# Optimization experiments

Measured on AMD Instinct MI355X. Metric: run time of the kernel, lower is better.

Reference implementation:

```python
import jax, jax.numpy as jnp
import numpy as np


def gru_step(x, h, W, U, b):
    # Keras GRU, reset_after=True. W:[in,3H] U:[H,3H] b:[2,3H]
    gi = x @ W + b[0]
    gh = h @ U + b[1]
    iz, ir, ih = jnp.split(gi, 3, axis=-1)
    hz, hr, hh = jnp.split(gh, 3, axis=-1)
    z = jax.nn.sigmoid(iz + hz)
    r = jax.nn.sigmoid(ir + hr)
    n = jnp.tanh(ih + r * hh)
    return z * h + (1.0 - z) * n


def gru_seq(x, W, U, b):
    # x: [B,S,in] -> outputs [B,S,H], last state [B,H]; zero initial state
    B = x.shape[0]
    H = U.shape[0]
    h0 = jnp.zeros((B, H), x.dtype)
    def step(h, xt):
        h2 = gru_step(xt, h, W, U, b)
        return h2, h2
    hT, ys = jax.lax.scan(step, h0, jnp.swapaxes(x, 0, 1))
    return jnp.swapaxes(ys, 0, 1), hT


def setup_inputs() -> dict:
    key = jax.random.key(0)
    ks = jax.random.split(key, 24)
    V_en, V_fr, E, H = 32000, 32000, 256, 1024
    B, S = 32, 48
    s = 0.05
    d = {}
    d["inputs"] = jax.random.randint(ks[0], (B, S), 0, V_en, dtype=jnp.int32)
    d["gen_seq_len"] = 32
    d["start_id"] = 1
    d["emb_en"] = jax.random.normal(ks[1], (V_en, E), jnp.float32) * s
    d["emb_fr"] = jax.random.normal(ks[2], (V_fr, E), jnp.float32) * s
    # encoder GRUs: layer0 in=E, layer1 in=H
    d["enc_W0"] = jax.random.normal(ks[3], (E, 3 * H), jnp.float32) * s
    d["enc_U0"] = jax.random.normal(ks[4], (H, 3 * H), jnp.float32) * s
    d["enc_b0"] = jnp.zeros((2, 3 * H), jnp.float32)
    d["enc_W1"] = jax.random.normal(ks[5], (H, 3 * H), jnp.float32) * s
    d["enc_U1"] = jax.random.normal(ks[6], (H, 3 * H), jnp.float32) * s
    d["enc_b1"] = jnp.zeros((2, 3 * H), jnp.float32)
    # decoder GRUs: layer0 in = H(context)+E(embed), layer1 in = H
    d["dec_W0"] = jax.random.normal(ks[7], (H + E, 3 * H), jnp.float32) * s
    d["dec_U0"] = jax.random.normal(ks[8], (H, 3 * H), jnp.float32) * s
    d["dec_b0"] = jnp.zeros((2, 3 * H), jnp.float32)
    d["dec_W1"] = jax.random.normal(ks[9], (H, 3 * H), jnp.float32) * s
    d["dec_U1"] = jax.random.normal(ks[10], (H, 3 * H), jnp.float32) * s
    d["dec_b1"] = jnp.zeros((2, 3 * H), jnp.float32)
    # Bahdanau attention
    d["attn_W1"] = jax.random.normal(ks[11], (H, H), jnp.float32) * s
    d["attn_b1"] = jnp.zeros((H,), jnp.float32)
    d["attn_W2"] = jax.random.normal(ks[12], (H, H), jnp.float32) * s
    d["attn_b2"] = jnp.zeros((H,), jnp.float32)
    d["attn_V"] = jax.random.normal(ks[13], (H, 1), jnp.float32) * s
    d["attn_Vb"] = jnp.zeros((1,), jnp.float32)
    # output projection
    d["fc_W"] = jax.random.normal(ks[14], (H, V_fr), jnp.float32) * s
    d["fc_b"] = jnp.zeros((V_fr,), jnp.float32)
    return d


def reference(inputs, gen_seq_len, start_id, emb_en, emb_fr,
              enc_W0, enc_U0, enc_b0, enc_W1, enc_U1, enc_b1,
              dec_W0, dec_U0, dec_b0, dec_W1, dec_U1, dec_b1,
              attn_W1, attn_b1, attn_W2, attn_b2, attn_V, attn_Vb,
              fc_W, fc_b):
    B = inputs.shape[0]
    H = enc_U0.shape[0]
    V_fr = fc_W.shape[1]
    # ---- encoder ----
    x = emb_en[inputs]                       # [B,S,E]
    x, _ = gru_seq(x, enc_W0, enc_U0, enc_b0)
    enc_out, enc_hidden = gru_seq(x, enc_W1, enc_U1, enc_b1)  # [B,S,H], [B,H]
    # precompute W2(values) (same math as recomputing per step)
    enc_proj = enc_out @ attn_W2 + attn_b2   # [B,S,H]
    zeros_h = jnp.zeros((B, H), jnp.float32)

    def dec_step(carry, _):
        dec_in, hidden = carry
        # Bahdanau attention
        q = hidden @ attn_W1 + attn_b1                          # [B,H]
        score = jnp.tanh(q[:, None, :] + enc_proj) @ attn_V + attn_Vb  # [B,S,1]
        w = jax.nn.softmax(score, axis=1)
        ctx = jnp.sum(w * enc_out, axis=1)                      # [B,H]
        xt = jnp.concatenate([ctx, emb_fr[dec_in]], axis=-1)    # [B,H+E]
        # decoder GRUs with state reset to zero each step (initial_state=None)
        h1 = gru_step(xt, zeros_h, dec_W0, dec_U0, dec_b0)
        h2 = gru_step(h1, zeros_h, dec_W1, dec_U1, dec_b1)
        logits = h2 @ fc_W + fc_b                               # [B,V_fr]
        nxt = jnp.argmax(logits, axis=1).astype(jnp.int32)
        return (nxt, h2), logits

    dec_in0 = jnp.full((B,), start_id, dtype=jnp.int32)
    (_, _), logits_seq = jax.lax.scan(dec_step, (dec_in0, enc_hidden),
                                      None, length=gen_seq_len - 1)
    first = jax.nn.one_hot(dec_in0, V_fr, dtype=jnp.float32)[:, None, :]
    return jnp.concatenate([first, jnp.swapaxes(logits_seq, 0, 1)], axis=1)
```

## Files before the change

### kernel.cpp

```cpp
#include <hip/hip_runtime.h>
#include <math.h>

#define BB 32
#define SS 48
#define HH 1024
#define EE 256
#define VOC 32000
#define GEN 32
#define G3 3072
#define CH 256
#define NLOG (VOC / 128)

typedef float v4f __attribute__((ext_vector_type(4)));

__device__ __forceinline__ float sigf(float x) { return 1.f / (1.f + expf(-x)); }

__global__ __launch_bounds__(256) void embed_en_k(const int* __restrict__ inputs,
                                                  const float* __restrict__ emb,
                                                  float* __restrict__ x) {
    int i = blockIdx.x * 256 + threadIdx.x;
    int row = i >> 8;
    int e = i & 255;
    x[i] = emb[(size_t)inputs[row] * EE + e];
}

__global__ __launch_bounds__(256) void transpose_k(const float* __restrict__ U,
                                                   float* __restrict__ UT,
                                                   int R, int C) {
    __shared__ float t[32][33];
    int tx = threadIdx.x & 31, ty = threadIdx.x >> 5;
    int bx = blockIdx.x * 32;
    int by = blockIdx.y * 32;
#pragma unroll
    for (int i = 0; i < 4; ++i)
        t[ty + 8 * i][tx] = U[(size_t)(by + ty + 8 * i) * C + bx + tx];
    __syncthreads();
#pragma unroll
    for (int i = 0; i < 4; ++i)
        UT[(size_t)(bx + ty + 8 * i) * R + by + tx] = t[tx][ty + 8 * i];
}

__global__ __launch_bounds__(256) void gemm64(const float* __restrict__ A,
                                              const float* __restrict__ Bm,
                                              const float* __restrict__ bias,
                                              float* __restrict__ C,
                                              int N, int K) {
    __shared__ float As[32][68];
    __shared__ float Bs[32][68];
    int tid = threadIdx.x;
    int tx = tid & 15, ty = tid >> 4;
    int arow = blockIdx.y * 64, bcol = blockIdx.x * 64;
    int am = tid >> 2;
    int aq = tid & 3;
    int bk = tid >> 4;
    int bn = tid & 15;
    float acc[4][4] = {};
    for (int k0 = 0; k0 < K; k0 += 32) {
        float4 a0 = *(const float4*)(A + (size_t)(arow + am) * K + k0 + aq * 8);
        float4 a1 = *(const float4*)(A + (size_t)(arow + am) * K + k0 + aq * 8 + 4);
        float4 b0 = *(const float4*)(Bm + (size_t)(k0 + bk) * N + bcol + bn * 4);
        float4 b1 = *(const float4*)(Bm + (size_t)(k0 + bk + 16) * N + bcol + bn * 4);
        __syncthreads();
        As[aq * 8 + 0][am] = a0.x; As[aq * 8 + 1][am] = a0.y;
        As[aq * 8 + 2][am] = a0.z; As[aq * 8 + 3][am] = a0.w;
        As[aq * 8 + 4][am] = a1.x; As[aq * 8 + 5][am] = a1.y;
        As[aq * 8 + 6][am] = a1.z; As[aq * 8 + 7][am] = a1.w;
        *(float4*)&Bs[bk][bn * 4] = b0;
        *(float4*)&Bs[bk + 16][bn * 4] = b1;
        __syncthreads();
#pragma unroll
        for (int kk = 0; kk < 32; ++kk) {
            float4 a = *(const float4*)&As[kk][ty * 4];
            float4 b = *(const float4*)&Bs[kk][tx * 4];
            acc[0][0] += a.x * b.x; acc[0][1] += a.x * b.y;
            acc[0][2] += a.x * b.z; acc[0][3] += a.x * b.w;
            acc[1][0] += a.y * b.x; acc[1][1] += a.y * b.y;
            acc[1][2] += a.y * b.z; acc[1][3] += a.y * b.w;
            acc[2][0] += a.z * b.x; acc[2][1] += a.z * b.y;
            acc[2][2] += a.z * b.z; acc[2][3] += a.z * b.w;
            acc[3][0] += a.w * b.x; acc[3][1] += a.w * b.y;
            acc[3][2] += a.w * b.z; acc[3][3] += a.w * b.w;
        }
    }
    float4 bb = *(const float4*)&bias[bcol + tx * 4];
#pragma unroll
    for (int i = 0; i < 4; ++i) {
        size_t row = arow + ty * 4 + i;
        *(float4*)(C + row * N + bcol + tx * 4) =
            make_float4(acc[i][0] + bb.x, acc[i][1] + bb.y,
                        acc[i][2] + bb.z, acc[i][3] + bb.w);
    }
}

__global__ __launch_bounds__(384) void enc_step(
    const float* __restrict__ gi,
    const float* __restrict__ UT,
    const float* __restrict__ b1,
    const float* __restrict__ hin,
    float* __restrict__ hout,
    float* __restrict__ seqout,
    int t) {
    __shared__ float hs[32][260];
    __shared__ float ghs[12][33];
    const int tid = threadIdx.x;
    const int c0 = blockIdx.x * 4;
    const int ks = tid & 31;
    const int outIdx = tid >> 5;
    const int cq = outIdx >> 2;
    const int mo = outIdx & 3;
    const float* Ubase = UT + (size_t)(cq * HH + c0) * HH;
    float acc[4][8];
#pragma unroll
    for (int a = 0; a < 4; ++a)
#pragma unroll
        for (int b = 0; b < 8; ++b) acc[a][b] = 0.f;
    for (int ch = 0; ch < HH / CH; ++ch) {
        for (int i = tid; i < 32 * 64; i += 384) {
            int m = i >> 6, q = i & 63;
            *(float4*)&hs[m][q * 4] =
                *(const float4*)&hin[m * HH + ch * CH + q * 4];
        }
        __syncthreads();
#pragma unroll
        for (int j = 0; j < 2; ++j) {
            int kq = (j * 32 + ks) * 4;
            float4 uv[4];
#pragma unroll
            for (int ci = 0; ci < 4; ++ci)
                uv[ci] = *(const float4*)&Ubase[(size_t)ci * HH + ch * CH + kq];
#pragma unroll
            for (int mi = 0; mi < 8; ++mi) {
                float4 hv = *(const float4*)&hs[mo * 8 + mi][kq];
#pragma unroll
                for (int ci = 0; ci < 4; ++ci)
                    acc[ci][mi] += hv.x * uv[ci].x + hv.y * uv[ci].y +
                                   hv.z * uv[ci].z + hv.w * uv[ci].w;
            }
        }
        __syncthreads();
    }
#pragma unroll
    for (int ci = 0; ci < 4; ++ci)
#pragma unroll
        for (int mi = 0; mi < 8; ++mi) {
            float v = acc[ci][mi];
            v += __shfl_xor(v, 1, 64);
            v += __shfl_xor(v, 2, 64);
            v += __shfl_xor(v, 4, 64);
            v += __shfl_xor(v, 8, 64);
            v += __shfl_xor(v, 16, 64);
            if (ks == 0) ghs[cq * 4 + ci][mo * 8 + mi] = v;
        }
    __syncthreads();
    if (tid < 128) {
        int m = tid & 31, c = tid >> 5;
        int col = c0 + c;
        float ghz = ghs[c][m] + b1[col];
        float ghr = ghs[4 + c][m] + b1[HH + col];
        float ghh = ghs[8 + c][m] + b1[2 * HH + col];
        const float* gir = gi + ((size_t)m * SS + t) * G3;
        float z = sigf(gir[col] + ghz);
        float r = sigf(gir[HH + col] + ghr);
        float nn = tanhf(gir[2 * HH + col] + r * ghh);
        float h = z * hin[m * HH + col] + (1.f - z) * nn;
        hout[m * HH + col] = h;
        seqout[((size_t)m * SS + t) * HH + col] = h;
    }
}

__global__ __launch_bounds__(384) void dec_step(
    const float* __restrict__ xt, int K,
    const float* __restrict__ WT,
    const float* __restrict__ b0, const float* __restrict__ b1,
    float* __restrict__ hout) {
    __shared__ float hs[32][260];
    __shared__ float ghs[12][33];
    const int tid = threadIdx.x;
    const int c0 = blockIdx.x * 4;
    const int ks = tid & 31;
    const int outIdx = tid >> 5;
    const int cq = outIdx >> 2;
    const int mo = outIdx & 3;
    const float* Ubase = WT + (size_t)(cq * HH + c0) * K;
    float acc[4][8];
#pragma unroll
    for (int a = 0; a < 4; ++a)
#pragma unroll
        for (int b = 0; b < 8; ++b) acc[a][b] = 0.f;
    const int nch = K / CH;
    for (int ch = 0; ch < nch; ++ch) {
        for (int i = tid; i < 32 * 64; i += 384) {
            int m = i >> 6, q = i & 63;
            *(float4*)&hs[m][q * 4] =
                *(const float4*)&xt[(size_t)m * K + ch * CH + q * 4];
        }
        __syncthreads();
#pragma unroll
        for (int j = 0; j < 2; ++j) {
            int kq = (j * 32 + ks) * 4;
            float4 uv[4];
#pragma unroll
            for (int ci = 0; ci < 4; ++ci)
                uv[ci] = *(const float4*)&Ubase[(size_t)ci * K + ch * CH + kq];
#pragma unroll
            for (int mi = 0; mi < 8; ++mi) {
                float4 hv = *(const float4*)&hs[mo * 8 + mi][kq];
#pragma unroll
                for (int ci = 0; ci < 4; ++ci)
                    acc[ci][mi] += hv.x * uv[ci].x + hv.y * uv[ci].y +
                                   hv.z * uv[ci].z + hv.w * uv[ci].w;
            }
        }
        __syncthreads();
    }
#pragma unroll
    for (int ci = 0; ci < 4; ++ci)
#pragma unroll
        for (int mi = 0; mi < 8; ++mi) {
            float v = acc[ci][mi];
            v += __shfl_xor(v, 1, 64);
            v += __shfl_xor(v, 2, 64);
            v += __shfl_xor(v, 4, 64);
            v += __shfl_xor(v, 8, 64);
            v += __shfl_xor(v, 16, 64);
            if (ks == 0) ghs[cq * 4 + ci][mo * 8 + mi] = v;
        }
    __syncthreads();
    if (tid < 128) {
        int m = tid & 31, c = tid >> 5;
        int col = c0 + c;
        float z = sigf(ghs[c][m] + b0[col] + b1[col]);
        float r = sigf(ghs[4 + c][m] + b0[HH + col] + b1[HH + col]);
        float nn = tanhf(ghs[8 + c][m] + b0[2 * HH + col] + r * b1[2 * HH + col]);
        hout[m * HH + col] = (1.f - z) * nn;
    }
}

__global__ __launch_bounds__(384) void dec_front(
    const float* __restrict__ qb, const float* __restrict__ encP,
    const float* __restrict__ vvec, const float* __restrict__ vb,
    const float* __restrict__ emb_fr, const int* __restrict__ start_id,
    const float* __restrict__ pmv, const int* __restrict__ pmi, int nb,
    const float* __restrict__ P, const float* __restrict__ W0,
    const float* __restrict__ b0, const float* __restrict__ b1,
    float* __restrict__ h1out) {
    __shared__ float sc[SS];
    __shared__ float wsm[SS];
    __shared__ float sv[256];
    __shared__ int si[256];
    __shared__ int stok;
    __shared__ float embl[EE];
    __shared__ float g[3][128];
    const int tid = threadIdx.x;
    const int b = blockIdx.x & 31;
    const int j0 = (blockIdx.x >> 5) * 128;
    const int wave = tid >> 6, lane = tid & 63;
    if (nb == 0) {
        if (tid == 0) stok = start_id[0];
    } else {
        if (tid < 256) {
            float best = -3.4e38f; int bi = 0x7fffffff;
            for (int i = tid; i < nb; i += 256) {
                float v = pmv[(size_t)b * nb + i];
                int ix = pmi[(size_t)b * nb + i];
                if (v > best || (v == best && ix < bi)) { best = v; bi = ix; }
            }
            sv[tid] = best; si[tid] = bi;
        }
        __syncthreads();
        for (int s = 128; s; s >>= 1) {
            if (tid < s) {
                if (sv[tid + s] > sv[tid] ||
                    (sv[tid + s] == sv[tid] && si[tid + s] < si[tid])) {
                    sv[tid] = sv[tid + s]; si[tid] = si[tid + s];
                }
            }
            __syncthreads();
        }
        if (tid == 0) stok = si[0];
    }
    __syncthreads();
    if (tid < EE) embl[tid] = emb_fr[(size_t)stok * EE + tid];
    const float* q = qb + (size_t)b * HH;
    for (int s = wave; s < SS; s += 6) {
        const float* ep = encP + (size_t)(b * SS + s) * HH;
        float sum = 0.f;
        for (int h = lane; h < HH; h += 64)
            sum += tanhf(q[h] + ep[h]) * vvec[h];
#pragma unroll
        for (int o = 32; o; o >>= 1) sum += __shfl_xor(sum, o, 64);
        if (lane == 0) sc[s] = sum + vb[0];
    }
    __syncthreads();
    if (tid < 64) {
        float v = (lane < SS) ? sc[lane] : -3.4e38f;
        float m = v;
#pragma unroll
        for (int o = 32; o; o >>= 1) m = fmaxf(m, __shfl_xor(m, o, 64));
        float e = (lane < SS) ? expf(v - m) : 0.f;
        float ssum = e;
#pragma unroll
        for (int o = 32; o; o >>= 1) ssum += __shfl_xor(ssum, o, 64);
        if (lane < SS) wsm[lane] = e / ssum;
    }
    __syncthreads();
    {
        int gate = tid >> 7;
        int col = tid & 127;
        int gcol = gate * HH + j0 + col;
        float acc = b0[gcol];
        const float* Pb = P + (size_t)b * SS * G3 + gcol;
#pragma unroll 8
        for (int s = 0; s < SS; ++s) acc += wsm[s] * Pb[(size_t)s * G3];
        const float* Wb = W0 + (size_t)HH * G3 + gcol;
#pragma unroll 8
        for (int k = 0; k < EE; ++k) acc += embl[k] * Wb[(size_t)k * G3];
        g[gate][col] = acc;
    }
    __syncthreads();
    if (tid < 128) {
        int jj = j0 + tid;
        float z = sigf(g[0][tid] + b1[jj]);
        float r = sigf(g[1][tid] + b1[HH + jj]);
        float nn = tanhf(g[2][tid] + r * b1[2 * HH + jj]);
        h1out[(size_t)b * HH + jj] = (1.f - z) * nn;
    }
}

__global__ __launch_bounds__(256) void logits_q(const float* __restrict__ A,
                                                const float* __restrict__ fcW,
                                                const float* __restrict__ fcb,
                                                float* __restrict__ Cl,
                                                const float* __restrict__ qW,
                                                const float* __restrict__ qb,
                                                float* __restrict__ Cq,
                                                float* __restrict__ pmv,
                                                int* __restrict__ pmi,
                                                int qonly) {
    __shared__ float As[32][36];
    __shared__ float Bs[32][132];
    int tid = threadIdx.x;
    int bid = blockIdx.x;
    bool isq = qonly || (bid >= NLOG);
    const float* Bm = isq ? qW : fcW;
    const float* bias = isq ? qb : fcb;
    float* C = isq ? Cq : Cl;
    int N = isq ? HH : VOC;
    int ldc = isq ? HH : GEN * VOC;
    int bcol = (isq ? (qonly ? bid : bid - NLOG) : bid) * 128;
    int nc = tid & 15, mg = (tid >> 4) & 7, ksl = tid >> 7;
    const int nch = HH / 32;
    int am = tid >> 3, aq = tid & 7;
    float4 ra = *(const float4*)(A + (size_t)am * HH + aq * 4);
    float4 rb[4];
#pragma unroll
    for (int it = 0; it < 4; ++it) {
        int lin = it * 256 + tid;
        int k = lin >> 5, q = lin & 31;
        const float* p = Bm + (size_t)k * N + bcol + q * 4;
        if (isq) { rb[it] = *(const float4*)p; }
        else { v4f v = __builtin_nontemporal_load((const v4f*)p); rb[it] = *(float4*)&v; }
    }
    float acc[4][8] = {};
    for (int ch = 0; ch < nch; ++ch) {
        __syncthreads();
        As[aq * 4 + 0][am] = ra.x; As[aq * 4 + 1][am] = ra.y;
        As[aq * 4 + 2][am] = ra.z; As[aq * 4 + 3][am] = ra.w;
#pragma unroll
        for (int it = 0; it < 4; ++it) {
            int lin = it * 256 + tid;
            int k = lin >> 5, q = lin & 31;
            *(float4*)&Bs[k][q * 4] = rb[it];
        }
        __syncthreads();
        if (ch + 1 < nch) {
            int k0 = (ch + 1) * 32;
            ra = *(const float4*)(A + (size_t)am * HH + k0 + aq * 4);
#pragma unroll
            for (int it = 0; it < 4; ++it) {
                int lin = it * 256 + tid;
                int k = lin >> 5, q = lin & 31;
                const float* p = Bm + (size_t)(k0 + k) * N + bcol + q * 4;
                if (isq) { rb[it] = *(const float4*)p; }
                else { v4f v = __builtin_nontemporal_load((const v4f*)p); rb[it] = *(float4*)&v; }
            }
        }
#pragma unroll
        for (int kk = 0; kk < 16; ++kk) {
            int k2 = kk * 2 + ksl;
            float a[4], b[8];
            *(float4*)&a[0] = *(const float4*)&As[k2][mg * 4];
            *(float4*)&b[0] = *(const float4*)&Bs[k2][nc * 8];
            *(float4*)&b[4] = *(const float4*)&Bs[k2][nc * 8 + 4];
#pragma unroll
            for (int r = 0; r < 4; ++r)
#pragma unroll
                for (int j = 0; j < 8; ++j) acc[r][j] += a[r] * b[j];
        }
    }
    __syncthreads();
    float* red = &Bs[0][0];
    if (ksl == 1) {
        int p = tid & 127;
#pragma unroll
        for (int r = 0; r < 4; ++r)
#pragma unroll
            for (int j = 0; j < 8; ++j) red[p * 32 + r * 8 + j] = acc[r][j];
    }
    __syncthreads();
    if (ksl == 0) {
        int p = tid;
#pragma unroll
        for (int r = 0; r < 4; ++r)
#pragma unroll
            for (int j = 0; j < 8; ++j) acc[r][j] += red[p * 32 + r * 8 + j];
        float bb[8];
        *(float4*)&bb[0] = *(const float4*)&bias[bcol + nc * 8];
        *(float4*)&bb[4] = *(const float4*)&bias[bcol + nc * 8 + 4];
#pragma unroll
        for (int r = 0; r < 4; ++r) {
#pragma unroll
            for (int j = 0; j < 8; ++j) acc[r][j] += bb[j];
            int row = mg * 4 + r;
            float* cp = C + (size_t)row * ldc + bcol + nc * 8;
            if (isq) {
                *(float4*)cp = make_float4(acc[r][0], acc[r][1], acc[r][2], acc[r][3]);
                *(float4*)(cp + 4) = make_float4(acc[r][4], acc[r][5], acc[r][6], acc[r][7]);
            } else {
                v4f o0 = {acc[r][0], acc[r][1], acc[r][2], acc[r][3]};
                v4f o1 = {acc[r][4], acc[r][5], acc[r][6], acc[r][7]};
                __builtin_nontemporal_store(o0, (v4f*)cp);
                __builtin_nontemporal_store(o1, (v4f*)(cp + 4));
            }
        }
        if (!isq) {
#pragma unroll
            for (int r = 0; r < 4; ++r) {
                float best = acc[r][0]; int bidx = bcol + nc * 8;
#pragma unroll
                for (int j = 1; j < 8; ++j)
                    if (acc[r][j] > best) { best = acc[r][j]; bidx = bcol + nc * 8 + j; }
#pragma unroll
                for (int o = 1; o < 16; o <<= 1) {
                    float pv = __shfl_xor(best, o, 64);
                    int pi = __shfl_xor(bidx, o, 64);
                    if (pv > best || (pv == best && pi < bidx)) { best = pv; bidx = pi; }
                }
                if (nc == 0) {
                    int row = mg * 4 + r;
                    pmv[row * NLOG + bid] = best;
                    pmi[row * NLOG + bid] = bidx;
                }
            }
        }
    }
}

__global__ __launch_bounds__(256) void init_dec(float* __restrict__ out,
                                                const int* __restrict__ start_id) {
    int idx = blockIdx.x * 256 + threadIdx.x;
    int sid = start_id[0];
    int b = idx / VOC, v = idx % VOC;
    out[(size_t)b * (GEN * VOC) + v] = (v == sid) ? 1.f : 0.f;
}

extern "C" void kernel_launch(void* const* d_in, const int* in_sizes, int n_in,
                              void* d_out, int out_size, void* d_ws, size_t ws_size,
                              hipStream_t stream) {
    const int*   inputs   = (const int*)d_in[0];
    const int*   start_id = (const int*)d_in[2];
    const float* emb_en   = (const float*)d_in[3];
    const float* emb_fr   = (const float*)d_in[4];
    const float* enc_W0   = (const float*)d_in[5];
    const float* enc_U0   = (const float*)d_in[6];
    const float* enc_b0   = (const float*)d_in[7];
    const float* enc_W1   = (const float*)d_in[8];
    const float* enc_U1   = (const float*)d_in[9];
    const float* enc_b1   = (const float*)d_in[10];
    const float* dec_W0   = (const float*)d_in[11];
    const float* dec_b0   = (const float*)d_in[13];
    const float* dec_W1   = (const float*)d_in[14];
    const float* dec_b1   = (const float*)d_in[16];
    const float* attn_W1  = (const float*)d_in[17];
    const float* attn_b1  = (const float*)d_in[18];
    const float* attn_W2  = (const float*)d_in[19];
    const float* attn_b2  = (const float*)d_in[20];
    const float* attn_V   = (const float*)d_in[21];
    const float* attn_Vb  = (const float*)d_in[22];
    const float* fc_W     = (const float*)d_in[23];
    const float* fc_b     = (const float*)d_in[24];
    float* out = (float*)d_out;
    float* ws  = (float*)d_ws;

    float* giA   = ws;
    float* x_emb = giA + (size_t)BB * SS * G3;
    float* seq0  = x_emb + (size_t)BB * SS * EE;
    float* encO  = seq0 + (size_t)BB * SS * HH;
    float* encP  = encO + (size_t)BB * SS * HH;
    float* h0A   = encP + (size_t)BB * SS * HH;
    float* h0B   = h0A + BB * HH;
    float* h1A   = h0B + BB * HH;
    float* h1B   = h1A + BB * HH;
    float* qbuf  = h1B + BB * HH;
    float* h1buf = qbuf + BB * HH;
    float* pmv   = h1buf + BB * HH;
    int*   pmi   = (int*)(pmv + 32 * NLOG);
    float* U0T   = (float*)(pmi + 32 * NLOG);
    float* U1T   = U0T + (size_t)G3 * HH;
    float* Pmat  = giA;
    float* W1Td  = U0T;
    float* zb    = h1B;

    embed_en_k<<<(BB * SS * EE) / 256, 256, 0, stream>>>(inputs, emb_en, x_emb);
    gemm64<<<dim3(G3 / 64, (BB * SS) / 64), 256, 0, stream>>>(
        x_emb, enc_W0, enc_b0, giA, G3, EE);
    transpose_k<<<dim3(96, 32), 256, 0, stream>>>(enc_U0, U0T, HH, G3);
    transpose_k<<<dim3(96, 32), 256, 0, stream>>>(enc_U1, U1T, HH, G3);
    hipMemsetAsync(h0A, 0, BB * HH * sizeof(float), stream);
    for (int t = 0; t < SS; ++t) {
        const float* hin = (t & 1) ? h0B : h0A;
        float* hout = (t & 1) ? h0A : h0B;
        enc_step<<<256, 384, 0, stream>>>(giA, U0T, enc_b0 + G3, hin, hout, seq0, t);
    }
    gemm64<<<dim3(G3 / 64, (BB * SS) / 64), 256, 0, stream>>>(
        seq0, enc_W1, enc_b1, giA, G3, HH);
    hipMemsetAsync(h1A, 0, BB * HH * sizeof(float), stream);
    for (int t = 0; t < SS; ++t) {
        const float* hin = (t & 1) ? h1B : h1A;
        float* hout = (t & 1) ? h1A : h1B;
        enc_step<<<256, 384, 0, stream>>>(giA, U1T, enc_b1 + G3, hin, hout, encO, t);
    }
    gemm64<<<dim3(HH / 64, (BB * SS) / 64), 256, 0, stream>>>(
        encO, attn_W2, attn_b2, encP, HH, HH);

    transpose_k<<<dim3(96, 32), 256, 0, stream>>>(dec_W1, W1Td, HH, G3);
    hipMemsetAsync(zb, 0, G3 * sizeof(float), stream);
    gemm64<<<dim3(G3 / 64, (BB * SS) / 64), 256, 0, stream>>>(
        encO, dec_W0, zb, Pmat, G3, HH);

    init_dec<<<(BB * VOC) / 256, 256, 0, stream>>>(out, start_id);
    logits_q<<<HH / 128, 256, 0, stream>>>(h1A, fc_W, fc_b, out,
                                           attn_W1, attn_b1, qbuf, pmv, pmi, 1);
    for (int step = 1; step < GEN; ++step) {
        dec_front<<<256, 384, 0, stream>>>(qbuf, encP, attn_V, attn_Vb,
                                           emb_fr, start_id, pmv, pmi,
                                           (step == 1) ? 0 : NLOG,
                                           Pmat, dec_W0, dec_b0, dec_b0 + G3,
                                           h1buf);
        dec_step<<<256, 384, 0, stream>>>(h1buf, HH, W1Td, dec_b1,
                                          dec_b1 + G3, h1A);
        logits_q<<<NLOG + HH / 128, 256, 0, stream>>>(h1A, fc_W, fc_b,
                                                      out + (size_t)step * VOC,
                                                      attn_W1, attn_b1, qbuf,
                                                      pmv, pmi, 0);
    }
}
```

Before: 6.995 ms.

## Split logits GEMM into 64-column tiles with 4-way K split and double-buffered prefetch

The vocabulary logits path now uses 64-column tiles, which doubles the block count to 500 and gives better CU coverage on the 32000-wide fc_W stream. Each block splits K four ways and reduces the partial sums through padded shared memory. Register prefetch now runs two chunks ahead to hide more of the global load latency. The attention-query path keeps the old 128-column tiling, and the per-block argmax partials grow to 500 entries per row for dec_front to scan.

```diff
diff --git a/kernel.cpp b/kernel.cpp
--- a/kernel.cpp
+++ b/kernel.cpp
@@ -9,7 +9,7 @@
 #define GEN 32
 #define G3 3072
 #define CH 256
-#define NLOG (VOC / 128)
+#define NL64 (VOC / 64)
 
 typedef float v4f __attribute__((ext_vector_type(4)));
 
@@ -337,120 +337,203 @@
                                                 float* __restrict__ pmv,
                                                 int* __restrict__ pmi,
                                                 int qonly) {
-    __shared__ float As[32][36];
-    __shared__ float Bs[32][132];
+    __shared__ float smem[6336];
     int tid = threadIdx.x;
     int bid = blockIdx.x;
-    bool isq = qonly || (bid >= NLOG);
-    const float* Bm = isq ? qW : fcW;
-    const float* bias = isq ? qb : fcb;
-    float* C = isq ? Cq : Cl;
-    int N = isq ? HH : VOC;
-    int ldc = isq ? HH : GEN * VOC;
-    int bcol = (isq ? (qonly ? bid : bid - NLOG) : bid) * 128;
-    int nc = tid & 15, mg = (tid >> 4) & 7, ksl = tid >> 7;
-    const int nch = HH / 32;
-    int am = tid >> 3, aq = tid & 7;
-    float4 ra = *(const float4*)(A + (size_t)am * HH + aq * 4);
-    float4 rb[4];
-#pragma unroll
-    for (int it = 0; it < 4; ++it) {
-        int lin = it * 256 + tid;
-        int k = lin >> 5, q = lin & 31;
-        const float* p = Bm + (size_t)k * N + bcol + q * 4;
-        if (isq) { rb[it] = *(const float4*)p; }
-        else { v4f v = __builtin_nontemporal_load((const v4f*)p); rb[it] = *(float4*)&v; }
-    }
-    float acc[4][8] = {};
-    for (int ch = 0; ch < nch; ++ch) {
-        __syncthreads();
-        As[aq * 4 + 0][am] = ra.x; As[aq * 4 + 1][am] = ra.y;
-        As[aq * 4 + 2][am] = ra.z; As[aq * 4 + 3][am] = ra.w;
-#pragma unroll
-        for (int it = 0; it < 4; ++it) {
+    bool isq = qonly || (bid >= NL64);
+    if (!isq) {
+        float* As = smem;
+        float* Bs = smem + 1152;
+        int bcol = bid * 64;
+        int nc = tid & 7, mg = (tid >> 3) & 7, ksl = tid >> 6;
+        int am = tid >> 3, aq = tid & 7;
+        float4 ra, ra2, rb[2], rb2[2];
+        ra = *(const float4*)(A + (size_t)am * HH + aq * 4);
+        ra2 = *(const float4*)(A + (size_t)am * HH + 32 + aq * 4);
+#pragma unroll
+        for (int it = 0; it < 2; ++it) {
             int lin = it * 256 + tid;
-            int k = lin >> 5, q = lin & 31;
-            *(float4*)&Bs[k][q * 4] = rb[it];
-        }
-        __syncthreads();
-        if (ch + 1 < nch) {
-            int k0 = (ch + 1) * 32;
-            ra = *(const float4*)(A + (size_t)am * HH + k0 + aq * 4);
-#pragma unroll
-            for (int it = 0; it < 4; ++it) {
+            int bk = lin >> 4, bq = lin & 15;
+            v4f v = __builtin_nontemporal_load(
+                (const v4f*)(fcW + (size_t)bk * VOC + bcol + bq * 4));
+            rb[it] = *(float4*)&v;
+        }
+#pragma unroll
+        for (int it = 0; it < 2; ++it) {
+            int lin = it * 256 + tid;
+            int bk = lin >> 4, bq = lin & 15;
+            v4f v = __builtin_nontemporal_load(
+                (const v4f*)(fcW + (size_t)(32 + bk) * VOC + bcol + bq * 4));
+            rb2[it] = *(float4*)&v;
+        }
+        float acc[4][8] = {};
+        for (int ch = 0; ch < HH / 32; ++ch) {
+            __syncthreads();
+            As[(aq * 4 + 0) * 36 + am] = ra.x;
+            As[(aq * 4 + 1) * 36 + am] = ra.y;
+            As[(aq * 4 + 2) * 36 + am] = ra.z;
+            As[(aq * 4 + 3) * 36 + am] = ra.w;
+#pragma unroll
+            for (int it = 0; it < 2; ++it) {
                 int lin = it * 256 + tid;
-                int k = lin >> 5, q = lin & 31;
-                const float* p = Bm + (size_t)(k0 + k) * N + bcol + q * 4;
-                if (isq) { rb[it] = *(const float4*)p; }
-                else { v4f v = __builtin_nontemporal_load((const v4f*)p); rb[it] = *(float4*)&v; }
-            }
-        }
-#pragma unroll
-        for (int kk = 0; kk < 16; ++kk) {
-            int k2 = kk * 2 + ksl;
-            float a[4], b[8];
-            *(float4*)&a[0] = *(const float4*)&As[k2][mg * 4];
-            *(float4*)&b[0] = *(const float4*)&Bs[k2][nc * 8];
-            *(float4*)&b[4] = *(const float4*)&Bs[k2][nc * 8 + 4];
+                int bk = lin >> 4, bq = lin & 15;
+                *(float4*)&Bs[bk * 68 + bq * 4] = rb[it];
+            }
+            __syncthreads();
+            ra = ra2;
+            rb[0] = rb2[0]; rb[1] = rb2[1];
+            if (ch + 2 < HH / 32) {
+                int k0 = (ch + 2) * 32;
+                ra2 = *(const float4*)(A + (size_t)am * HH + k0 + aq * 4);
+#pragma unroll
+                for (int it = 0; it < 2; ++it) {
+                    int lin = it * 256 + tid;
+                    int bk = lin >> 4, bq = lin & 15;
+                    v4f v = __builtin_nontemporal_load(
+                        (const v4f*)(fcW + (size_t)(k0 + bk) * VOC + bcol + bq * 4));
+                    rb2[it] = *(float4*)&v;
+                }
+            }
+#pragma unroll
+            for (int kk = 0; kk < 8; ++kk) {
+                int k2 = kk * 4 + ksl;
+                float a[4], b[8];
+                *(float4*)&a[0] = *(const float4*)&As[k2 * 36 + mg * 4];
+                *(float4*)&b[0] = *(const float4*)&Bs[k2 * 68 + nc * 8];
+                *(float4*)&b[4] = *(const float4*)&Bs[k2 * 68 + nc * 8 + 4];
+#pragma unroll
+                for (int r = 0; r < 4; ++r)
+#pragma unroll
+                    for (int j = 0; j < 8; ++j) acc[r][j] += a[r] * b[j];
+            }
+        }
+        __syncthreads();
+        if (ksl) {
+            int p = ((ksl - 1) * 64 + (tid & 63)) * 33;
 #pragma unroll
             for (int r = 0; r < 4; ++r)
 #pragma unroll
-                for (int j = 0; j < 8; ++j) acc[r][j] += a[r] * b[j];
-        }
-    }
-    __syncthreads();
-    float* red = &Bs[0][0];
-    if (ksl == 1) {
-        int p = tid & 127;
-#pragma unroll
-        for (int r = 0; r < 4; ++r)
-#pragma unroll
-            for (int j = 0; j < 8; ++j) red[p * 32 + r * 8 + j] = acc[r][j];
-    }
-    __syncthreads();
-    if (ksl == 0) {
-        int p = tid;
-#pragma unroll
-        for (int r = 0; r < 4; ++r)
-#pragma unroll
-            for (int j = 0; j < 8; ++j) acc[r][j] += red[p * 32 + r * 8 + j];
-        float bb[8];
-        *(float4*)&bb[0] = *(const float4*)&bias[bcol + nc * 8];
-        *(float4*)&bb[4] = *(const float4*)&bias[bcol + nc * 8 + 4];
-#pragma unroll
-        for (int r = 0; r < 4; ++r) {
-#pragma unroll
-            for (int j = 0; j < 8; ++j) acc[r][j] += bb[j];
-            int row = mg * 4 + r;
-            float* cp = C + (size_t)row * ldc + bcol + nc * 8;
-            if (isq) {
-                *(float4*)cp = make_float4(acc[r][0], acc[r][1], acc[r][2], acc[r][3]);
-                *(float4*)(cp + 4) = make_float4(acc[r][4], acc[r][5], acc[r][6], acc[r][7]);
-            } else {
+                for (int j = 0; j < 8; ++j) smem[p + r * 8 + j] = acc[r][j];
+        }
+        __syncthreads();
+        if (ksl == 0) {
+#pragma unroll
+            for (int s = 0; s < 3; ++s) {
+                int p = (s * 64 + tid) * 33;
+#pragma unroll
+                for (int r = 0; r < 4; ++r)
+#pragma unroll
+                    for (int j = 0; j < 8; ++j) acc[r][j] += smem[p + r * 8 + j];
+            }
+            float bb[8];
+            *(float4*)&bb[0] = *(const float4*)&fcb[bcol + nc * 8];
+            *(float4*)&bb[4] = *(const float4*)&fcb[bcol + nc * 8 + 4];
+#pragma unroll
+            for (int r = 0; r < 4; ++r) {
+#pragma unroll
+                for (int j = 0; j < 8; ++j) acc[r][j] += bb[j];
+                int row = mg * 4 + r;
+                float* cp = Cl + (size_t)row * (GEN * VOC) + bcol + nc * 8;
                 v4f o0 = {acc[r][0], acc[r][1], acc[r][2], acc[r][3]};
                 v4f o1 = {acc[r][4], acc[r][5], acc[r][6], acc[r][7]};
                 __builtin_nontemporal_store(o0, (v4f*)cp);
                 __builtin_nontemporal_store(o1, (v4f*)(cp + 4));
-            }
-        }
-        if (!isq) {
-#pragma unroll
-            for (int r = 0; r < 4; ++r) {
                 float best = acc[r][0]; int bidx = bcol + nc * 8;
 #pragma unroll
                 for (int j = 1; j < 8; ++j)
                     if (acc[r][j] > best) { best = acc[r][j]; bidx = bcol + nc * 8 + j; }
 #pragma unroll
-                for (int o = 1; o < 16; o <<= 1) {
+                for (int o = 1; o < 8; o <<= 1) {
                     float pv = __shfl_xor(best, o, 64);
                     int pi = __shfl_xor(bidx, o, 64);
                     if (pv > best || (pv == best && pi < bidx)) { best = pv; bidx = pi; }
                 }
                 if (nc == 0) {
-                    int row = mg * 4 + r;
-                    pmv[row * NLOG + bid] = best;
-                    pmi[row * NLOG + bid] = bidx;
+                    pmv[row * NL64 + bid] = best;
+                    pmi[row * NL64 + bid] = bidx;
                 }
+            }
+        }
+        return;
+    }
+    {
+        float* As = smem;
+        float* Bs = smem + 1152;
+        int bcol = (qonly ? bid : bid - NL64) * 128;
+        int nc = tid & 15, mg = (tid >> 4) & 7, ksl = tid >> 7;
+        int am = tid >> 3, aq = tid & 7;
+        float4 ra = *(const float4*)(A + (size_t)am * HH + aq * 4);
+        float4 rb[4];
+#pragma unroll
+        for (int it = 0; it < 4; ++it) {
+            int lin = it * 256 + tid;
+            int k = lin >> 5, q = lin & 31;
+            rb[it] = *(const float4*)(qW + (size_t)k * HH + bcol + q * 4);
+        }
+        float acc[4][8] = {};
+        for (int ch = 0; ch < HH / 32; ++ch) {
+            __syncthreads();
+            As[(aq * 4 + 0) * 36 + am] = ra.x;
+            As[(aq * 4 + 1) * 36 + am] = ra.y;
+            As[(aq * 4 + 2) * 36 + am] = ra.z;
+            As[(aq * 4 + 3) * 36 + am] = ra.w;
+#pragma unroll
+            for (int it = 0; it < 4; ++it) {
+                int lin = it * 256 + tid;
+                int k = lin >> 5, q = lin & 31;
+                *(float4*)&Bs[k * 132 + q * 4] = rb[it];
+            }
+            __syncthreads();
+            if (ch + 1 < HH / 32) {
+                int k0 = (ch + 1) * 32;
+                ra = *(const float4*)(A + (size_t)am * HH + k0 + aq * 4);
+#pragma unroll
+                for (int it = 0; it < 4; ++it) {
+                    int lin = it * 256 + tid;
+                    int k = lin >> 5, q = lin & 31;
+                    rb[it] = *(const float4*)(qW + (size_t)(k0 + k) * HH + bcol + q * 4);
+                }
+            }
+#pragma unroll
+            for (int kk = 0; kk < 16; ++kk) {
+                int k2 = kk * 2 + ksl;
+                float a[4], b[8];
+                *(float4*)&a[0] = *(const float4*)&As[k2 * 36 + mg * 4];
+                *(float4*)&b[0] = *(const float4*)&Bs[k2 * 132 + nc * 8];
+                *(float4*)&b[4] = *(const float4*)&Bs[k2 * 132 + nc * 8 + 4];
+#pragma unroll
+                for (int r = 0; r < 4; ++r)
+#pragma unroll
+                    for (int j = 0; j < 8; ++j) acc[r][j] += a[r] * b[j];
+            }
+        }
+        __syncthreads();
+        float* red = Bs;
+        if (ksl == 1) {
+            int p = tid & 127;
+#pragma unroll
+            for (int r = 0; r < 4; ++r)
+#pragma unroll
+                for (int j = 0; j < 8; ++j) red[p * 32 + r * 8 + j] = acc[r][j];
+        }
+        __syncthreads();
+        if (ksl == 0) {
+            int p = tid;
+#pragma unroll
+            for (int r = 0; r < 4; ++r)
+#pragma unroll
+                for (int j = 0; j < 8; ++j) acc[r][j] += red[p * 32 + r * 8 + j];
+            float bb[8];
+            *(float4*)&bb[0] = *(const float4*)&qb[bcol + nc * 8];
+            *(float4*)&bb[4] = *(const float4*)&qb[bcol + nc * 8 + 4];
+#pragma unroll
+            for (int r = 0; r < 4; ++r) {
+#pragma unroll
+                for (int j = 0; j < 8; ++j) acc[r][j] += bb[j];
+                int row = mg * 4 + r;
+                float* cp = Cq + (size_t)row * HH + bcol + nc * 8;
+                *(float4*)cp = make_float4(acc[r][0], acc[r][1], acc[r][2], acc[r][3]);
+                *(float4*)(cp + 4) = make_float4(acc[r][4], acc[r][5], acc[r][6], acc[r][7]);
             }
         }
     }
@@ -504,8 +587,8 @@
     float* qbuf  = h1B + BB * HH;
     float* h1buf = qbuf + BB * HH;
     float* pmv   = h1buf + BB * HH;
-    int*   pmi   = (int*)(pmv + 32 * NLOG);
-    float* U0T   = (float*)(pmi + 32 * NLOG);
+    int*   pmi   = (int*)(pmv + 32 * NL64);
+    float* U0T   = (float*)(pmi + 32 * NL64);
     float* U1T   = U0T + (size_t)G3 * HH;
     float* Pmat  = giA;
     float* W1Td  = U0T;
@@ -544,12 +627,12 @@
     for (int step = 1; step < GEN; ++step) {
         dec_front<<<256, 384, 0, stream>>>(qbuf, encP, attn_V, attn_Vb,
                                            emb_fr, start_id, pmv, pmi,
-                                           (step == 1) ? 0 : NLOG,
+                                           (step == 1) ? 0 : NL64,
                                            Pmat, dec_W0, dec_b0, dec_b0 + G3,
                                            h1buf);
         dec_step<<<256, 384, 0, stream>>>(h1buf, HH, W1Td, dec_b1,
                                           dec_b1 + G3, h1A);
-        logits_q<<<NLOG + HH / 128, 256, 0, stream>>>(h1A, fc_W, fc_b,
+        logits_q<<<NL64 + HH / 128, 256, 0, stream>>>(h1A, fc_W, fc_b,
                                                       out + (size_t)step * VOC,
                                                       attn_W1, attn_b1, qbuf,
                                                       pmv, pmi, 0);
```

Result: slower. 7.404 ms (+5.8%).
